# Kernel optimization log

Hardware: AMD Instinct MI355X
Metric: run time of the kernel (lower is better)

Reference implementation:

```python
import jax, jax.numpy as jnp
import numpy as np

NUM_EXPERTS = 8
IN_FEATURES = 2048
OUT_FEATURES = 5632
GROUP_SIZE = 64
NUM_TOKENS = 4096


def setup_inputs() -> dict:
    key = jax.random.key(0)
    k1, k2, k3, k4 = jax.random.split(key, 4)
    inp = jax.random.normal(k1, (NUM_TOKENS, IN_FEATURES), dtype=jnp.float32)
    # tokens are pre-sorted contiguously per expert; balanced routing
    tokens_per_expert = jnp.full((NUM_EXPERTS,), NUM_TOKENS // NUM_EXPERTS, dtype=jnp.int32)
    # int4 quantized weights stored as integer codes in [0, 16)
    weights = jax.random.randint(k2, (NUM_EXPERTS, IN_FEATURES, OUT_FEATURES), 0, 16, dtype=jnp.int32)
    n_groups = IN_FEATURES // GROUP_SIZE
    scales = jax.random.uniform(k3, (NUM_EXPERTS, n_groups, OUT_FEATURES, 1), dtype=jnp.float32,
                                minval=0.005, maxval=0.02)
    zeros = jax.random.normal(k4, (NUM_EXPERTS, n_groups, OUT_FEATURES, 1), dtype=jnp.float32) * 0.01
    scales_and_zeros = jnp.concatenate([scales, zeros], axis=-1)  # [E, K//G, N, 2]
    return {"input": inp, "tokens_per_expert": tokens_per_expert,
            "weights": weights, "scales_and_zeros": scales_and_zeros}


def _dequant(weights, scales_and_zeros):
    # torchao int4 convention: w = (q - 8) * scale + zero, grouped along K
    E, K, N = weights.shape
    n_groups = scales_and_zeros.shape[1]
    g = K // n_groups
    q = weights.astype(jnp.float32).reshape(E, n_groups, g, N)
    s = scales_and_zeros[..., 0][:, :, None, :]  # [E, K//G, 1, N]
    z = scales_and_zeros[..., 1][:, :, None, :]
    return ((q - 8.0) * s + z).reshape(E, K, N)


def reference(input, tokens_per_expert, weights, scales_and_zeros):
    num_tokens, K = input.shape
    E = weights.shape[0]
    W = _dequant(weights, scales_and_zeros)  # [E, K, N] float32
    # expert id of each (contiguous-sorted) token from cumsum boundaries
    cum = jnp.cumsum(tokens_per_expert)                      # [E]
    seg = jnp.searchsorted(cum, jnp.arange(num_tokens), side='right')  # [T]
    start = jnp.concatenate([jnp.zeros((1,), cum.dtype), cum[:-1]])
    pos = jnp.arange(num_tokens) - start[seg]                # slot within expert block
    # capacity-based grouped GEMM (balanced routing in setup: C = T // E)
    C = num_tokens // E
    buf = jnp.zeros((E, C, K), input.dtype).at[seg, pos].set(input)
    y = jnp.einsum('eck,ekn->ecn', buf, W)                   # per-expert GEMM
    return y[seg, pos]                                       # [T, N]
```

## Files before the change

kernel.cpp:

```cpp
#include <hip/hip_runtime.h>

#define NE    8
#define KDIM  2048
#define NDIM  5632
#define NTOK  4096
#define CAP   512
#define NGRP  32
#define BM    128
#define BN    128
#define BK    32
#define MT    4
#define NT    44

#define NBT   44
#define TRB   (NE * NGRP * NBT)
#define ACV_BLOCKS  (NTOK * KDIM / (8 * 256))
#define PS    134

#define WT_BYTES  ((size_t)NE * KDIM * NDIM * 2)
#define ABF_BYTES ((size_t)NTOK * KDIM * 2)

typedef __attribute__((ext_vector_type(8))) short bf16x8;
typedef __attribute__((ext_vector_type(4))) short bf16x4;
typedef __attribute__((ext_vector_type(4))) float f32x4;

typedef __attribute__((address_space(3))) unsigned int* lds_p;
typedef const __attribute__((address_space(1))) unsigned int* glb_p;

static __device__ __forceinline__ void ld16(const void* g, void* l) {
    __builtin_amdgcn_global_load_lds((glb_p)g, (lds_p)l, 16, 0, 0);
}

static __device__ __forceinline__ unsigned short f2bf(float f) {
    union { float f; unsigned u; } x; x.f = f;
    return (unsigned short)((x.u + 0x7fffu + ((x.u >> 16) & 1u)) >> 16);
}

__global__ __launch_bounds__(256)
void prep_kernel(const int* __restrict__ wq, const float* __restrict__ inp,
                 const float* __restrict__ sz,
                 unsigned short* __restrict__ wt, unsigned short* __restrict__ abf)
{
    const int bid = blockIdx.x;
    if (bid < TRB) {
        const int e  = bid / (NGRP * NBT);
        const int r  = bid % (NGRP * NBT);
        const int g  = r / NBT;
        const int nb = r % NBT;
        __shared__ unsigned short T[64 * PS];
        const int t = threadIdx.x;

        const int n4    = (t & 31) * 4;
        const int r0    = t >> 5;
        const int nglob = nb * 128 + n4;
        const float* szp = sz + ((size_t)(e * NGRP + g) * NDIM + nglob) * 2;
        const float4 sz01 = *(const float4*)szp;
        const float4 sz23 = *(const float4*)(szp + 4);
        const float s0 = sz01.x, z0 = sz01.y - 8.f * sz01.x;
        const float s1 = sz01.z, z1 = sz01.w - 8.f * sz01.z;
        const float s2 = sz23.x, z2 = sz23.y - 8.f * sz23.x;
        const float s3 = sz23.z, z3 = sz23.w - 8.f * sz23.z;
        const int* cbase = wq + (size_t)(e * KDIM + g * 64) * NDIM + nglob;
        #pragma unroll
        for (int ri = 0; ri < 8; ++ri) {
            const int row = r0 + ri * 8;
            const int4 c = *(const int4*)(cbase + (size_t)row * NDIM);
            unsigned p0 = (unsigned)f2bf(fmaf((float)c.x, s0, z0))
                        | ((unsigned)f2bf(fmaf((float)c.y, s1, z1)) << 16);
            unsigned p1 = (unsigned)f2bf(fmaf((float)c.z, s2, z2))
                        | ((unsigned)f2bf(fmaf((float)c.w, s3, z3)) << 16);
            unsigned* dst = (unsigned*)&T[row * PS + n4];
            dst[0] = p0; dst[1] = p1;
        }
        __syncthreads();

        const int kq = t & 7;
        #pragma unroll
        for (int it = 0; it < 4; ++it) {
            const int n = it * 32 + (t >> 3);
            bf16x8 v;
            #pragma unroll
            for (int i = 0; i < 8; ++i)
                v[i] = (short)T[(kq * 8 + i) * PS + n];
            unsigned short* dp = wt + ((size_t)e * NDIM + nb * 128 + n) * KDIM
                                    + g * 64 + kq * 8;
            *(bf16x8*)dp = v;
        }
    } else {
        const size_t t = (size_t)(bid - TRB) * 256 + threadIdx.x;
        const float4* p = (const float4*)inp + t * 2;
        const float4 v0 = p[0], v1 = p[1];
        bf16x8 h;
        h[0] = (short)f2bf(v0.x); h[1] = (short)f2bf(v0.y);
        h[2] = (short)f2bf(v0.z); h[3] = (short)f2bf(v0.w);
        h[4] = (short)f2bf(v1.x); h[5] = (short)f2bf(v1.y);
        h[6] = (short)f2bf(v1.z); h[7] = (short)f2bf(v1.w);
        *((bf16x8*)abf + t) = h;
    }
}

__global__ __launch_bounds__(256)
void hqq_gemm3(const unsigned short* __restrict__ abf,
               const unsigned short* __restrict__ wt,
               float* __restrict__ out)
{
    const int bid = blockIdx.x;
    const int e   = bid / (MT * NT);
    const int rem = bid % (MT * NT);
    const int nt  = rem >> 2;
    const int mt  = rem & 3;

    __shared__ __align__(16) unsigned short Alds[BM * BK];
    __shared__ __align__(16) unsigned short Blds[BN * BK];

    const int tid  = threadIdx.x;
    const int wave = tid >> 6;
    const int lane = tid & 63;
    const int m0   = e * CAP + mt * BM;
    const int n0   = nt * BN;

    const int srow = wave * 32 + (lane >> 2);
    const int skq  = lane & 3;
    const unsigned short* Ag0 = abf + (size_t)(m0 + srow) * KDIM + skq * 8;
    const unsigned short* Ag1 = Ag0 + (size_t)16 * KDIM;
    const unsigned short* Bg0 = wt + ((size_t)e * NDIM + n0 + srow) * KDIM + skq * 8;
    const unsigned short* Bg1 = Bg0 + (size_t)16 * KDIM;
    unsigned short* Al0 = &Alds[wave * 1024];
    unsigned short* Al1 = &Alds[wave * 1024 + 512];
    unsigned short* Bl0 = &Blds[wave * 1024];
    unsigned short* Bl1 = &Blds[wave * 1024 + 512];

    f32x4 acc[4][4];
    #pragma unroll
    for (int i = 0; i < 4; ++i)
        #pragma unroll
        for (int j = 0; j < 4; ++j)
            acc[i][j] = (f32x4){0.f, 0.f, 0.f, 0.f};

    const int wm = (wave >> 1) << 6;
    const int wn = (wave & 1) << 6;
    const int lr = lane & 15;
    const int lq = lane >> 4;

    for (int kk = 0; kk < KDIM / BK; ++kk) {
        ld16(Ag0, Al0);
        ld16(Ag1, Al1);
        ld16(Bg0, Bl0);
        ld16(Bg1, Bl1);
        Ag0 += BK; Ag1 += BK; Bg0 += BK; Bg1 += BK;
        __syncthreads();

        bf16x8 af[4], bfv[4];
        #pragma unroll
        for (int i = 0; i < 4; ++i)
            af[i] = *(const bf16x8*)&Alds[(wm + i * 16 + lr) * BK + lq * 8];
        #pragma unroll
        for (int j = 0; j < 4; ++j)
            bfv[j] = *(const bf16x8*)&Blds[(wn + j * 16 + lr) * BK + lq * 8];
        #pragma unroll
        for (int i = 0; i < 4; ++i)
            #pragma unroll
            for (int j = 0; j < 4; ++j)
                acc[i][j] = __builtin_amdgcn_mfma_f32_16x16x32_bf16(af[i], bfv[j], acc[i][j], 0, 0, 0);

        __syncthreads();
    }

    const int orow0 = m0 + wm + lq * 4;
    const int ocol0 = n0 + wn + lr;
    #pragma unroll
    for (int i = 0; i < 4; ++i)
        #pragma unroll
        for (int r = 0; r < 4; ++r) {
            float* op = out + (size_t)(orow0 + i * 16 + r) * NDIM + ocol0;
            #pragma unroll
            for (int j = 0; j < 4; ++j)
                op[j * 16] = acc[i][j][r];
        }
}

#define LDSS  40
__global__ __launch_bounds__(256, 2)
void hqq_gemm_fallback(const float* __restrict__ inp,
                       const int*   __restrict__ wq,
                       const float* __restrict__ sz,
                       float*       __restrict__ out)
{
    const int bid = blockIdx.x;
    const int e   = bid / (MT * NT);
    const int rem = bid % (MT * NT);
    const int nt  = rem >> 2;
    const int mt  = rem & 3;

    __shared__ __align__(16) short Alds[BM * LDSS];
    __shared__ __align__(16) short Blds[BN * LDSS];

    const int tid = threadIdx.x;
    const int m0  = e * CAP + mt * BM;
    const int n0  = nt * BN;

    const int a_kq  = tid & 7;
    const int a_row = tid >> 3;
    const int b_n   = tid & 127;
    const int b_h   = tid >> 7;

    const float* Ab  = inp + (size_t)m0 * KDIM;
    const int*   Wb  = wq  + (size_t)e * KDIM * NDIM + n0 + b_n;
    const float* SZb = sz  + (size_t)e * NGRP * (NDIM * 2) + (size_t)(n0 + b_n) * 2;

    f32x4 acc[4][4];
    #pragma unroll
    for (int i = 0; i < 4; ++i)
        #pragma unroll
        for (int j = 0; j < 4; ++j)
            acc[i][j] = (f32x4){0.f, 0.f, 0.f, 0.f};

    const int wave = tid >> 6;
    const int lane = tid & 63;
    const int wm = (wave >> 1) << 6;
    const int wn = (wave & 1) << 6;
    const int lr = lane & 15;
    const int lq = lane >> 4;

    for (int k0 = 0; k0 < KDIM; k0 += BK) {
        const int g = k0 >> 6;
        #pragma unroll
        for (int p = 0; p < 4; ++p) {
            const int row = a_row + p * 32;
            const float4 v = *(const float4*)(Ab + (size_t)row * KDIM + k0 + a_kq * 4);
            bf16x4 h;
            h[0] = (short)f2bf(v.x); h[1] = (short)f2bf(v.y);
            h[2] = (short)f2bf(v.z); h[3] = (short)f2bf(v.w);
            *(bf16x4*)&Alds[row * LDSS + a_kq * 4] = h;
        }
        const float2 s2 = *(const float2*)(SZb + (size_t)g * (NDIM * 2));
        const float s  = s2.x;
        const float z8 = s2.y - 8.f * s2.x;
        #pragma unroll
        for (int oo = 0; oo < 2; ++oo) {
            const int ko = b_h * 8 + oo * 16;
            const int* wp = Wb + (size_t)(k0 + ko) * NDIM;
            bf16x8 bb;
            #pragma unroll
            for (int j = 0; j < 8; ++j) {
                const float q = (float)wp[(size_t)j * NDIM];
                bb[j] = (short)f2bf(fmaf(q, s, z8));
            }
            *(bf16x8*)&Blds[b_n * LDSS + ko] = bb;
        }
        __syncthreads();
        bf16x8 af[4], bfv[4];
        #pragma unroll
        for (int i = 0; i < 4; ++i)
            af[i] = *(const bf16x8*)&Alds[(wm + i * 16 + lr) * LDSS + lq * 8];
        #pragma unroll
        for (int j = 0; j < 4; ++j)
            bfv[j] = *(const bf16x8*)&Blds[(wn + j * 16 + lr) * LDSS + lq * 8];
        #pragma unroll
        for (int i = 0; i < 4; ++i)
            #pragma unroll
            for (int j = 0; j < 4; ++j)
                acc[i][j] = __builtin_amdgcn_mfma_f32_16x16x32_bf16(af[i], bfv[j], acc[i][j], 0, 0, 0);
        __syncthreads();
    }

    const int orow0 = m0 + wm + lq * 4;
    const int ocol0 = n0 + wn + lr;
    #pragma unroll
    for (int i = 0; i < 4; ++i)
        #pragma unroll
        for (int r = 0; r < 4; ++r) {
            float* op = out + (size_t)(orow0 + i * 16 + r) * NDIM + ocol0;
            #pragma unroll
            for (int j = 0; j < 4; ++j)
                op[j * 16] = acc[i][j][r];
        }
}

extern "C" void kernel_launch(void* const* d_in, const int* in_sizes, int n_in,
                              void* d_out, int out_size, void* d_ws, size_t ws_size,
                              hipStream_t stream) {
    const float* inp = (const float*)d_in[0];
    const int*   wq  = (const int*)d_in[2];
    const float* sz  = (const float*)d_in[3];
    float*       out = (float*)d_out;

    if (ws_size >= WT_BYTES + ABF_BYTES) {
        unsigned short* wt  = (unsigned short*)d_ws;
        unsigned short* abf = (unsigned short*)((char*)d_ws + WT_BYTES);
        prep_kernel<<<dim3(TRB + ACV_BLOCKS), dim3(256), 0, stream>>>(wq, inp, sz, wt, abf);
        hqq_gemm3<<<dim3(NE * MT * NT), dim3(256), 0, stream>>>(abf, wt, out);
    } else {
        hqq_gemm_fallback<<<dim3(NE * MT * NT), dim3(256), 0, stream>>>(inp, wq, sz, out);
    }
}
```

Baseline: 719.8 us.

## Widen prep transpose tiles to 256-K rows and swizzle GEMM blocks across XCDs

The dequant/transpose prep kernel now handles 256 K-rows per block instead of 64, using dynamic LDS (about 66KB). Each output row segment is therefore written as 512 contiguous bytes rather than 128, which should make the bf16 weight writes better coalesced and cut block count. The GEMM block index is also remapped so that the four M-tiles sharing one weight N-tile run on the same XCD, aiming to improve L2 reuse of the B tile. The larger LDS footprint lowers prep occupancy, and the padding changes from 134 to 130, which may alter bank conflicts.

```diff
diff --git a/kernel.cpp b/kernel.cpp
--- a/kernel.cpp
+++ b/kernel.cpp
@@ -12,10 +12,12 @@
 #define MT    4
 #define NT    44
 
-#define NBT   44
-#define TRB   (NE * NGRP * NBT)
-#define ACV_BLOCKS  (NTOK * KDIM / (8 * 256))
-#define PS    134
+#define KB    (KDIM / 256)
+#define NB    (NDIM / 128)
+#define TRB2  (NE * KB * NB)
+#define ACV   (NTOK * KDIM / (8 * 256))
+#define PS    130
+#define PREP_LDS (256 * PS * 2)
 
 #define WT_BYTES  ((size_t)NE * KDIM * NDIM * 2)
 #define ABF_BYTES ((size_t)NTOK * KDIM * 2)
@@ -41,53 +43,59 @@
                  const float* __restrict__ sz,
                  unsigned short* __restrict__ wt, unsigned short* __restrict__ abf)
 {
+    extern __shared__ unsigned short T[];
     const int bid = blockIdx.x;
-    if (bid < TRB) {
-        const int e  = bid / (NGRP * NBT);
-        const int r  = bid % (NGRP * NBT);
-        const int g  = r / NBT;
-        const int nb = r % NBT;
-        __shared__ unsigned short T[64 * PS];
-        const int t = threadIdx.x;
+    if (bid < TRB2) {
+        const int e  = bid / (KB * NB);
+        const int r  = bid % (KB * NB);
+        const int kb = r / NB;
+        const int nb = r % NB;
+        const int t  = threadIdx.x;
 
         const int n4    = (t & 31) * 4;
         const int r0    = t >> 5;
         const int nglob = nb * 128 + n4;
-        const float* szp = sz + ((size_t)(e * NGRP + g) * NDIM + nglob) * 2;
-        const float4 sz01 = *(const float4*)szp;
-        const float4 sz23 = *(const float4*)(szp + 4);
-        const float s0 = sz01.x, z0 = sz01.y - 8.f * sz01.x;
-        const float s1 = sz01.z, z1 = sz01.w - 8.f * sz01.z;
-        const float s2 = sz23.x, z2 = sz23.y - 8.f * sz23.x;
-        const float s3 = sz23.z, z3 = sz23.w - 8.f * sz23.z;
-        const int* cbase = wq + (size_t)(e * KDIM + g * 64) * NDIM + nglob;
-        #pragma unroll
-        for (int ri = 0; ri < 8; ++ri) {
-            const int row = r0 + ri * 8;
-            const int4 c = *(const int4*)(cbase + (size_t)row * NDIM);
-            unsigned p0 = (unsigned)f2bf(fmaf((float)c.x, s0, z0))
-                        | ((unsigned)f2bf(fmaf((float)c.y, s1, z1)) << 16);
-            unsigned p1 = (unsigned)f2bf(fmaf((float)c.z, s2, z2))
-                        | ((unsigned)f2bf(fmaf((float)c.w, s3, z3)) << 16);
-            unsigned* dst = (unsigned*)&T[row * PS + n4];
-            dst[0] = p0; dst[1] = p1;
+        const int* cbase = wq + ((size_t)e * KDIM + kb * 256) * NDIM + nglob;
+        #pragma unroll
+        for (int gg = 0; gg < 4; ++gg) {
+            const float* szp = sz + ((size_t)(e * NGRP + kb * 4 + gg) * NDIM + nglob) * 2;
+            const float4 sz01 = *(const float4*)szp;
+            const float4 sz23 = *(const float4*)(szp + 4);
+            const float s0 = sz01.x, z0 = sz01.y - 8.f * sz01.x;
+            const float s1 = sz01.z, z1 = sz01.w - 8.f * sz01.z;
+            const float s2 = sz23.x, z2 = sz23.y - 8.f * sz23.x;
+            const float s3 = sz23.z, z3 = sz23.w - 8.f * sz23.z;
+            #pragma unroll
+            for (int rj = 0; rj < 8; ++rj) {
+                const int row = gg * 64 + rj * 8 + r0;
+                const int4 c = *(const int4*)(cbase + (size_t)row * NDIM);
+                unsigned p0 = (unsigned)f2bf(fmaf((float)c.x, s0, z0))
+                            | ((unsigned)f2bf(fmaf((float)c.y, s1, z1)) << 16);
+                unsigned p1 = (unsigned)f2bf(fmaf((float)c.z, s2, z2))
+                            | ((unsigned)f2bf(fmaf((float)c.w, s3, z3)) << 16);
+                unsigned* d = (unsigned*)&T[row * PS + n4];
+                d[0] = p0; d[1] = p1;
+            }
         }
         __syncthreads();
 
         const int kq = t & 7;
-        #pragma unroll
-        for (int it = 0; it < 4; ++it) {
-            const int n = it * 32 + (t >> 3);
-            bf16x8 v;
-            #pragma unroll
-            for (int i = 0; i < 8; ++i)
-                v[i] = (short)T[(kq * 8 + i) * PS + n];
-            unsigned short* dp = wt + ((size_t)e * NDIM + nb * 128 + n) * KDIM
-                                    + g * 64 + kq * 8;
-            *(bf16x8*)dp = v;
+        const int n0 = t >> 3;
+        #pragma unroll
+        for (int ni = 0; ni < 4; ++ni) {
+            const int n = n0 + ni * 32;
+            unsigned short* drow = wt + ((size_t)e * NDIM + nb * 128 + n) * KDIM + kb * 256;
+            #pragma unroll
+            for (int ko = 0; ko < 4; ++ko) {
+                bf16x8 v;
+                #pragma unroll
+                for (int i = 0; i < 8; ++i)
+                    v[i] = (short)T[(ko * 64 + kq * 8 + i) * PS + n];
+                *(bf16x8*)(drow + ko * 64 + kq * 8) = v;
+            }
         }
     } else {
-        const size_t t = (size_t)(bid - TRB) * 256 + threadIdx.x;
+        const size_t t = (size_t)(bid - TRB2) * 256 + threadIdx.x;
         const float4* p = (const float4*)inp + t * 2;
         const float4 v0 = p[0], v1 = p[1];
         bf16x8 h;
@@ -105,10 +113,13 @@
                float* __restrict__ out)
 {
     const int bid = blockIdx.x;
-    const int e   = bid / (MT * NT);
-    const int rem = bid % (MT * NT);
-    const int nt  = rem >> 2;
-    const int mt  = rem & 3;
+    const int xcd = bid & 7;
+    const int i5  = bid >> 3;
+    const int mt  = i5 & 3;
+    const int gi  = i5 >> 2;
+    const int g   = gi * 8 + xcd;
+    const int e   = g / NT;
+    const int nt  = g % NT;
 
     __shared__ __align__(16) unsigned short Alds[BM * BK];
     __shared__ __align__(16) unsigned short Blds[BN * BK];
@@ -288,7 +299,7 @@
     if (ws_size >= WT_BYTES + ABF_BYTES) {
         unsigned short* wt  = (unsigned short*)d_ws;
         unsigned short* abf = (unsigned short*)((char*)d_ws + WT_BYTES);
-        prep_kernel<<<dim3(TRB + ACV_BLOCKS), dim3(256), 0, stream>>>(wq, inp, sz, wt, abf);
+        prep_kernel<<<dim3(TRB2 + ACV), dim3(256), PREP_LDS, stream>>>(wq, inp, sz, wt, abf);
         hqq_gemm3<<<dim3(NE * MT * NT), dim3(256), 0, stream>>>(abf, wt, out);
     } else {
         hqq_gemm_fallback<<<dim3(NE * MT * NT), dim3(256), 0, stream>>>(inp, wq, sz, out);
```

After: 730.8 us. Within noise of the previous version (+1.5%).
